# Optimization experiments

Hardware: AMD Instinct MI355X
Metric: run time of the kernel (lower is better)

## Reference

```python
import jax, jax.numpy as jnp
import numpy as np

EPS = 1e-05

def conv1x1(x, W, b):
    # x: [B,C,H,W], W: [O,C], b: [O] -> [B,O,H,W]
    return jnp.einsum('oc,bchw->bohw', W, x) + b[None, :, None, None]

def setup_inputs() -> dict:
    key = jax.random.key(0)
    ks = jax.random.split(key, 11)
    C = 16
    B, H, W = 8, 512, 512
    s = 1.0 / np.sqrt(C)  # kaiming-ish fan-in scale for 1x1 convs
    inp = {'x': jax.random.normal(ks[0], (B, C, H, W), dtype=jnp.float32)}
    names = [('Wc', 'bc'), ('W1', 'b1'), ('W2', 'b2'), ('W3', 'b3'), ('W4', 'b4')]
    for i, (wn, bn) in enumerate(names):
        inp[wn] = jax.random.normal(ks[1 + 2 * i], (C, C), dtype=jnp.float32) * s
        inp[bn] = jax.random.normal(ks[2 + 2 * i], (C,), dtype=jnp.float32) * s
    return inp

def reference(x, Wc, bc, W1, b1, W2, b2, W3, b3, W4, b4):
    out1 = jnp.mean(x, axis=(2, 3), keepdims=True)          # adaptive avg pool (1,1)
    out3 = jnp.max(x, axis=(2, 3), keepdims=True)           # adaptive max pool (1,1)
    out2 = conv1x1(x, Wc, bc)
    out4 = conv1x1(x, W1, b1)
    wh = conv1x1(out2 / (out1 + EPS), W2, b2)
    wh_weight = jax.nn.sigmoid(jnp.tanh(wh))
    gray = conv1x1(out4 / (out3 + EPS), W3, b3)
    gray_weight = jax.nn.sigmoid(jnp.tanh(gray))
    out = conv1x1(x * (1.0 + wh_weight + gray_weight), W4, b4)
    return out
```

## Files before the change

kernel.cpp:

```cpp
#include <hip/hip_runtime.h>
#include <hip/hip_bf16.h>
#include <cmath>

#define HW 262144
#define NC 16
#define NB 8
#define NSEG 16
#define SEGSZ (HW / NSEG)
#define EPS 1e-5f

typedef float f32x4 __attribute__((ext_vector_type(4)));
typedef float f32x2 __attribute__((ext_vector_type(2)));
typedef short bf16x8 __attribute__((ext_vector_type(8)));

__global__ __launch_bounds__(256) void k_reduce(const float* __restrict__ x,
                                                float* __restrict__ psum,
                                                float* __restrict__ pmax) {
    int plane = blockIdx.x / NSEG;
    int seg   = blockIdx.x - plane * NSEG;
    const float4* p = reinterpret_cast<const float4*>(
        x + (size_t)plane * HW + (size_t)seg * SEGSZ);
    int t = threadIdx.x;
    float s = 0.0f, m = -INFINITY;
    #pragma unroll
    for (int it = 0; it < SEGSZ / (256 * 4); ++it) {
        float4 v = p[it * 256 + t];
        s += (v.x + v.y) + (v.z + v.w);
        m = fmaxf(m, fmaxf(fmaxf(v.x, v.y), fmaxf(v.z, v.w)));
    }
    #pragma unroll
    for (int off = 32; off > 0; off >>= 1) {
        s += __shfl_down(s, off, 64);
        m = fmaxf(m, __shfl_down(m, off, 64));
    }
    __shared__ float ls[4], lm[4];
    int wid = t >> 6, lane = t & 63;
    if (lane == 0) { ls[wid] = s; lm[wid] = m; }
    __syncthreads();
    if (t == 0) {
        psum[blockIdx.x] = (ls[0] + ls[1]) + (ls[2] + ls[3]);
        pmax[blockIdx.x] = fmaxf(fmaxf(lm[0], lm[1]), fmaxf(lm[2], lm[3]));
    }
}

__global__ __launch_bounds__(256) void k_params(
    const float* __restrict__ psum, const float* __restrict__ pmax,
    const float* __restrict__ Wc, const float* __restrict__ bc,
    const float* __restrict__ W1, const float* __restrict__ b1,
    const float* __restrict__ W2, const float* __restrict__ b2,
    const float* __restrict__ W3, const float* __restrict__ b3,
    const float* __restrict__ W4, const float* __restrict__ b4,
    float* __restrict__ params) {
    int b = blockIdx.x;
    int t = threadIdx.x;
    __shared__ float r2[NC], r4[NC], sWc[256], sW1[256], sW2[256], sW3[256];
    if (t < NC) {
        float s = 0.0f, m = -INFINITY;
        for (int k = 0; k < NSEG; ++k) {
            s += psum[(b * NC + t) * NSEG + k];
            m = fmaxf(m, pmax[(b * NC + t) * NSEG + k]);
        }
        r2[t] = 1.0f / (s * (1.0f / (float)HW) + EPS);
        r4[t] = 1.0f / (m + EPS);
    }
    sWc[t] = Wc[t]; sW1[t] = W1[t]; sW2[t] = W2[t]; sW3[t] = W3[t];
    __syncthreads();
    int o = t >> 4, i = t & 15;
    float accA = 0.0f, accG = 0.0f;
    #pragma unroll
    for (int c = 0; c < NC; ++c) {
        accA += sW2[o * NC + c] * r2[c] * sWc[c * NC + i];
        accG += sW3[o * NC + c] * r4[c] * sW1[c * NC + i];
    }
    float* P = params + b * 816;
    P[t]       = accA;
    P[256 + t] = accG;
    P[512 + t] = W4[t];
    if (i == 0) {
        float ba = 0.0f, bg = 0.0f;
        #pragma unroll
        for (int c = 0; c < NC; ++c) {
            ba += sW2[o * NC + c] * r2[c] * bc[c];
            bg += sW3[o * NC + c] * r4[c] * b1[c];
        }
        P[768 + o] = ba + b2[o];
        P[784 + o] = bg + b3[o];
        P[800 + o] = b4[o];
    }
}

__device__ __forceinline__ float gsig(float x) {
    float E = __expf(2.0f * x);
    float t = 1.0f - 2.0f * __builtin_amdgcn_rcpf(E + 1.0f);
    float t2 = t * t;
    return fmaf(t, fmaf(t2, fmaf(t2, 0.0020833333f, -0.0208333333f), 0.25f), 0.5f);
}

static __device__ __forceinline__ bf16x8 mk8(unsigned a, unsigned b,
                                             unsigned c, unsigned d) {
    union { unsigned u[4]; bf16x8 v; } r;
    r.u[0] = a; r.u[1] = b; r.u[2] = c; r.u[3] = d;
    return r.v;
}
static __device__ __forceinline__ unsigned pkhi(float x0, float x1) {
    return (__float_as_uint(x0) >> 16) | (__float_as_uint(x1) & 0xFFFF0000u);
}
static __device__ __forceinline__ float trunc_bf(float x) {
    return __uint_as_float(__float_as_uint(x) & 0xFFFF0000u);
}

static __device__ __forceinline__ f32x4 tile16(float x0, float x1, float x2, float x3,
                                               bf16x8 Af, bf16x8 Gf, bf16x8 Wf,
                                               f32x4 biasA, f32x4 biasG, f32x4 biasW) {
    unsigned vh01 = pkhi(x0, x1), vh23 = pkhi(x2, x3);
    unsigned vl01 = pkhi(x0 - trunc_bf(x0), x1 - trunc_bf(x1));
    unsigned vl23 = pkhi(x2 - trunc_bf(x2), x3 - trunc_bf(x3));
    bf16x8 B1 = mk8(vh01, vh23, vl01, vl23);
    bf16x8 B2 = mk8(vl01, vl23, vh01, vh23);
    f32x4 wh = __builtin_amdgcn_mfma_f32_16x16x32_bf16(Af, B1, biasA, 0, 0, 0);
    wh = __builtin_amdgcn_mfma_f32_16x16x32_bf16(Af, B2, wh, 0, 0, 0);
    f32x4 gr = __builtin_amdgcn_mfma_f32_16x16x32_bf16(Gf, B1, biasG, 0, 0, 0);
    float u0 = fmaf(x0, gsig(wh[0]) + gsig(gr[0]), x0);
    float u1 = fmaf(x1, gsig(wh[1]) + gsig(gr[1]), x1);
    float u2 = fmaf(x2, gsig(wh[2]) + gsig(gr[2]), x2);
    float u3 = fmaf(x3, gsig(wh[3]) + gsig(gr[3]), x3);
    unsigned uh01 = pkhi(u0, u1), uh23 = pkhi(u2, u3);
    unsigned ul01 = pkhi(u0 - trunc_bf(u0), u1 - trunc_bf(u1));
    unsigned ul23 = pkhi(u2 - trunc_bf(u2), u3 - trunc_bf(u3));
    f32x4 o = __builtin_amdgcn_mfma_f32_16x16x32_bf16(Wf, mk8(uh01, uh23, ul01, ul23), biasW, 0, 0, 0);
    o = __builtin_amdgcn_mfma_f32_16x16x32_bf16(Wf, mk8(ul01, ul23, uh01, uh23), o, 0, 0, 0);
    return o;
}

__global__ __launch_bounds__(256) void k_main(const float* __restrict__ x,
                                              const float* __restrict__ params,
                                              float* __restrict__ out) {
    int b    = blockIdx.x >> 8;
    int wib  = ((blockIdx.x & 255) << 2) + (threadIdx.x >> 6);
    int lane = threadIdx.x & 63;
    int m  = lane & 15;
    int kg = lane >> 4;

    const float* Pb = params + b * 816;

    f32x4 wa = *reinterpret_cast<const f32x4*>(Pb + m * 16 + kg * 4);
    f32x4 wg = *reinterpret_cast<const f32x4*>(Pb + 256 + m * 16 + kg * 4);
    f32x4 w4 = *reinterpret_cast<const f32x4*>(Pb + 512 + m * 16 + kg * 4);

    unsigned ah01 = pkhi(wa[0], wa[1]), ah23 = pkhi(wa[2], wa[3]);
    unsigned al01 = pkhi(wa[0] - trunc_bf(wa[0]), wa[1] - trunc_bf(wa[1]));
    unsigned al23 = pkhi(wa[2] - trunc_bf(wa[2]), wa[3] - trunc_bf(wa[3]));
    bf16x8 Af = mk8(ah01, ah23, al01, al23);

    unsigned g01 = pkhi(wg[0], wg[1]), g23 = pkhi(wg[2], wg[3]);
    bf16x8 Gf = mk8(g01, g23, g01, g23);

    unsigned w401 = pkhi(w4[0], w4[1]), w423 = pkhi(w4[2], w4[3]);
    unsigned wl01 = pkhi(w4[0] - trunc_bf(w4[0]), w4[1] - trunc_bf(w4[1]));
    unsigned wl23 = pkhi(w4[2] - trunc_bf(w4[2]), w4[3] - trunc_bf(w4[3]));
    bf16x8 Wf = mk8(w401, w423, wl01, wl23);

    f32x4 biasA = *reinterpret_cast<const f32x4*>(Pb + 768 + kg * 4);
    f32x4 biasG = *reinterpret_cast<const f32x4*>(Pb + 784 + kg * 4);
    f32x4 biasW = *reinterpret_cast<const f32x4*>(Pb + 800 + kg * 4);

    const f32x2* xb2 = reinterpret_cast<const f32x2*>(x + (size_t)b * NC * HW);
    f32x2*       ob2 = reinterpret_cast<f32x2*>(out + (size_t)b * NC * HW);

    unsigned basep = (unsigned)wib * 128 + (unsigned)m;
    unsigned off0 = (unsigned)(kg * 4 + 0) * (HW / 2) + basep;
    unsigned off1 = (unsigned)(kg * 4 + 1) * (HW / 2) + basep;
    unsigned off2 = (unsigned)(kg * 4 + 2) * (HW / 2) + basep;
    unsigned off3 = (unsigned)(kg * 4 + 3) * (HW / 2) + basep;

    #pragma unroll
    for (int t = 0; t < 8; ++t) {
        f32x2 v0 = xb2[off0 + t * 16];
        f32x2 v1 = xb2[off1 + t * 16];
        f32x2 v2 = xb2[off2 + t * 16];
        f32x2 v3 = xb2[off3 + t * 16];

        f32x4 oA = tile16(v0.x, v1.x, v2.x, v3.x, Af, Gf, Wf, biasA, biasG, biasW);
        f32x4 oB = tile16(v0.y, v1.y, v2.y, v3.y, Af, Gf, Wf, biasA, biasG, biasW);

        f32x2 s0; s0.x = oA[0]; s0.y = oB[0];
        f32x2 s1; s1.x = oA[1]; s1.y = oB[1];
        f32x2 s2; s2.x = oA[2]; s2.y = oB[2];
        f32x2 s3; s3.x = oA[3]; s3.y = oB[3];
        __builtin_nontemporal_store(s0, &ob2[off0 + t * 16]);
        __builtin_nontemporal_store(s1, &ob2[off1 + t * 16]);
        __builtin_nontemporal_store(s2, &ob2[off2 + t * 16]);
        __builtin_nontemporal_store(s3, &ob2[off3 + t * 16]);
    }
}

extern "C" void kernel_launch(void* const* d_in, const int* in_sizes, int n_in,
                              void* d_out, int out_size, void* d_ws, size_t ws_size,
                              hipStream_t stream) {
    const float* x  = (const float*)d_in[0];
    const float* Wc = (const float*)d_in[1];
    const float* bc = (const float*)d_in[2];
    const float* W1 = (const float*)d_in[3];
    const float* b1 = (const float*)d_in[4];
    const float* W2 = (const float*)d_in[5];
    const float* b2 = (const float*)d_in[6];
    const float* W3 = (const float*)d_in[7];
    const float* b3 = (const float*)d_in[8];
    const float* W4 = (const float*)d_in[9];
    const float* b4 = (const float*)d_in[10];
    float* out = (float*)d_out;

    float* psum   = (float*)d_ws;
    float* pmax   = psum + NB * NC * NSEG;
    float* params = pmax + NB * NC * NSEG;

    k_reduce<<<NB * NC * NSEG, 256, 0, stream>>>(x, psum, pmax);
    k_params<<<NB, 256, 0, stream>>>(psum, pmax, Wc, bc, W1, b1, W2, b2,
                                     W3, b3, W4, b4, params);
    k_main<<<NB * 256, 256, 0, stream>>>(x, params, out);
}
```

Before: 70.49 us.

## Fuse reduction, parameter setup and main pass into one cooperative kernel

Replaces the three-kernel pipeline with a single cooperative-launch kernel. Each block reduces its own slice of x, then a grid-wide sync runs, and each block recomputes the per-batch folded parameters before processing the same pixels it just reduced, which may help L2 reuse. Host-side occupancy and attribute queries run on every launch, and the grid barrier adds synchronisation cost. A fallback path fuses parameter computation into the main kernel, dropping the separate params kernel.

```diff
diff --git a/kernel.cpp b/kernel.cpp
--- a/kernel.cpp
+++ b/kernel.cpp
@@ -1,93 +1,22 @@
 #include <hip/hip_runtime.h>
-#include <hip/hip_bf16.h>
+#include <hip/hip_cooperative_groups.h>
 #include <cmath>
 
-#define HW 262144
-#define NC 16
-#define NB 8
+namespace cg = cooperative_groups;
+
+#define HW   262144
+#define NC   16
+#define NB   8
 #define NSEG 16
 #define SEGSZ (HW / NSEG)
-#define EPS 1e-5f
+#define NBLK 1024
+#define BPB  (NBLK / NB)
+#define PXB  (HW / BPB)
+#define EPS  1e-5f
 
 typedef float f32x4 __attribute__((ext_vector_type(4)));
 typedef float f32x2 __attribute__((ext_vector_type(2)));
 typedef short bf16x8 __attribute__((ext_vector_type(8)));
-
-__global__ __launch_bounds__(256) void k_reduce(const float* __restrict__ x,
-                                                float* __restrict__ psum,
-                                                float* __restrict__ pmax) {
-    int plane = blockIdx.x / NSEG;
-    int seg   = blockIdx.x - plane * NSEG;
-    const float4* p = reinterpret_cast<const float4*>(
-        x + (size_t)plane * HW + (size_t)seg * SEGSZ);
-    int t = threadIdx.x;
-    float s = 0.0f, m = -INFINITY;
-    #pragma unroll
-    for (int it = 0; it < SEGSZ / (256 * 4); ++it) {
-        float4 v = p[it * 256 + t];
-        s += (v.x + v.y) + (v.z + v.w);
-        m = fmaxf(m, fmaxf(fmaxf(v.x, v.y), fmaxf(v.z, v.w)));
-    }
-    #pragma unroll
-    for (int off = 32; off > 0; off >>= 1) {
-        s += __shfl_down(s, off, 64);
-        m = fmaxf(m, __shfl_down(m, off, 64));
-    }
-    __shared__ float ls[4], lm[4];
-    int wid = t >> 6, lane = t & 63;
-    if (lane == 0) { ls[wid] = s; lm[wid] = m; }
-    __syncthreads();
-    if (t == 0) {
-        psum[blockIdx.x] = (ls[0] + ls[1]) + (ls[2] + ls[3]);
-        pmax[blockIdx.x] = fmaxf(fmaxf(lm[0], lm[1]), fmaxf(lm[2], lm[3]));
-    }
-}
-
-__global__ __launch_bounds__(256) void k_params(
-    const float* __restrict__ psum, const float* __restrict__ pmax,
-    const float* __restrict__ Wc, const float* __restrict__ bc,
-    const float* __restrict__ W1, const float* __restrict__ b1,
-    const float* __restrict__ W2, const float* __restrict__ b2,
-    const float* __restrict__ W3, const float* __restrict__ b3,
-    const float* __restrict__ W4, const float* __restrict__ b4,
-    float* __restrict__ params) {
-    int b = blockIdx.x;
-    int t = threadIdx.x;
-    __shared__ float r2[NC], r4[NC], sWc[256], sW1[256], sW2[256], sW3[256];
-    if (t < NC) {
-        float s = 0.0f, m = -INFINITY;
-        for (int k = 0; k < NSEG; ++k) {
-            s += psum[(b * NC + t) * NSEG + k];
-            m = fmaxf(m, pmax[(b * NC + t) * NSEG + k]);
-        }
-        r2[t] = 1.0f / (s * (1.0f / (float)HW) + EPS);
-        r4[t] = 1.0f / (m + EPS);
-    }
-    sWc[t] = Wc[t]; sW1[t] = W1[t]; sW2[t] = W2[t]; sW3[t] = W3[t];
-    __syncthreads();
-    int o = t >> 4, i = t & 15;
-    float accA = 0.0f, accG = 0.0f;
-    #pragma unroll
-    for (int c = 0; c < NC; ++c) {
-        accA += sW2[o * NC + c] * r2[c] * sWc[c * NC + i];
-        accG += sW3[o * NC + c] * r4[c] * sW1[c * NC + i];
-    }
-    float* P = params + b * 816;
-    P[t]       = accA;
-    P[256 + t] = accG;
-    P[512 + t] = W4[t];
-    if (i == 0) {
-        float ba = 0.0f, bg = 0.0f;
-        #pragma unroll
-        for (int c = 0; c < NC; ++c) {
-            ba += sW2[o * NC + c] * r2[c] * bc[c];
-            bg += sW3[o * NC + c] * r4[c] * b1[c];
-        }
-        P[768 + o] = ba + b2[o];
-        P[784 + o] = bg + b3[o];
-        P[800 + o] = b4[o];
-    }
-}
 
 __device__ __forceinline__ float gsig(float x) {
     float E = __expf(2.0f * x);
@@ -132,66 +61,276 @@
     return o;
 }
 
-__global__ __launch_bounds__(256) void k_main(const float* __restrict__ x,
-                                              const float* __restrict__ params,
-                                              float* __restrict__ out) {
-    int b    = blockIdx.x >> 8;
-    int wib  = ((blockIdx.x & 255) << 2) + (threadIdx.x >> 6);
-    int lane = threadIdx.x & 63;
-    int m  = lane & 15;
-    int kg = lane >> 4;
-
-    const float* Pb = params + b * 816;
-
-    f32x4 wa = *reinterpret_cast<const f32x4*>(Pb + m * 16 + kg * 4);
-    f32x4 wg = *reinterpret_cast<const f32x4*>(Pb + 256 + m * 16 + kg * 4);
-    f32x4 w4 = *reinterpret_cast<const f32x4*>(Pb + 512 + m * 16 + kg * 4);
-
+template<int NITER>
+static __device__ __forceinline__ void phase3(const f32x2* __restrict__ xb2,
+                                              f32x2* __restrict__ ob2,
+                                              unsigned basep, int kg,
+                                              bf16x8 Af, bf16x8 Gf, bf16x8 Wf,
+                                              f32x4 biasA, f32x4 biasG, f32x4 biasW) {
+    unsigned off0 = (unsigned)(kg * 4 + 0) * (HW / 2) + basep;
+    unsigned off1 = (unsigned)(kg * 4 + 1) * (HW / 2) + basep;
+    unsigned off2 = (unsigned)(kg * 4 + 2) * (HW / 2) + basep;
+    unsigned off3 = (unsigned)(kg * 4 + 3) * (HW / 2) + basep;
+    #pragma unroll
+    for (int it = 0; it < NITER; ++it) {
+        f32x2 v0 = xb2[off0 + it * 16];
+        f32x2 v1 = xb2[off1 + it * 16];
+        f32x2 v2 = xb2[off2 + it * 16];
+        f32x2 v3 = xb2[off3 + it * 16];
+        f32x4 oA = tile16(v0.x, v1.x, v2.x, v3.x, Af, Gf, Wf, biasA, biasG, biasW);
+        f32x4 oB = tile16(v0.y, v1.y, v2.y, v3.y, Af, Gf, Wf, biasA, biasG, biasW);
+        f32x2 s0; s0.x = oA[0]; s0.y = oB[0];
+        f32x2 s1; s1.x = oA[1]; s1.y = oB[1];
+        f32x2 s2; s2.x = oA[2]; s2.y = oB[2];
+        f32x2 s3; s3.x = oA[3]; s3.y = oB[3];
+        __builtin_nontemporal_store(s0, &ob2[off0 + it * 16]);
+        __builtin_nontemporal_store(s1, &ob2[off1 + it * 16]);
+        __builtin_nontemporal_store(s2, &ob2[off2 + it * 16]);
+        __builtin_nontemporal_store(s3, &ob2[off3 + it * 16]);
+    }
+}
+
+__global__ __launch_bounds__(256) void k_reduce(const float* __restrict__ x,
+                                                float* __restrict__ psum,
+                                                float* __restrict__ pmax) {
+    int plane = blockIdx.x / NSEG;
+    int seg   = blockIdx.x - plane * NSEG;
+    const float4* p = reinterpret_cast<const float4*>(
+        x + (size_t)plane * HW + (size_t)seg * SEGSZ);
+    int t = threadIdx.x;
+    float s = 0.0f, m = -INFINITY;
+    #pragma unroll
+    for (int it = 0; it < SEGSZ / (256 * 4); ++it) {
+        float4 v = p[it * 256 + t];
+        s += (v.x + v.y) + (v.z + v.w);
+        m = fmaxf(m, fmaxf(fmaxf(v.x, v.y), fmaxf(v.z, v.w)));
+    }
+    #pragma unroll
+    for (int off = 32; off > 0; off >>= 1) {
+        s += __shfl_down(s, off, 64);
+        m = fmaxf(m, __shfl_down(m, off, 64));
+    }
+    __shared__ float ls[4], lm[4];
+    int wid = t >> 6, lane = t & 63;
+    if (lane == 0) { ls[wid] = s; lm[wid] = m; }
+    __syncthreads();
+    if (t == 0) {
+        psum[blockIdx.x] = (ls[0] + ls[1]) + (ls[2] + ls[3]);
+        pmax[blockIdx.x] = fmaxf(fmaxf(lm[0], lm[1]), fmaxf(lm[2], lm[3]));
+    }
+}
+
+__global__ __launch_bounds__(256) void k_main2(
+    const float* __restrict__ x,
+    const float* __restrict__ psum, const float* __restrict__ pmax,
+    const float* __restrict__ Wc, const float* __restrict__ bc,
+    const float* __restrict__ W1, const float* __restrict__ b1,
+    const float* __restrict__ W2, const float* __restrict__ b2,
+    const float* __restrict__ W3, const float* __restrict__ b3,
+    const float* __restrict__ W4, const float* __restrict__ b4,
+    float* __restrict__ out)
+{
+    int bid = blockIdx.x;
+    int b   = bid >> 8;
+    int t   = threadIdx.x;
+    int wave = t >> 6, lane = t & 63;
+
+    __shared__ float r2s[NC], r4s[NC];
+    __shared__ float sA[NC][17], sG[NC][17], sbias[48];
+
+    if (t < NC) {
+        const float* src = psum + (b * NC + t) * NSEG;
+        float s = 0.0f;
+        #pragma unroll
+        for (int k = 0; k < NSEG; ++k) s += src[k];
+        r2s[t] = 1.0f / (s * (1.0f / (float)HW) + EPS);
+    } else if (t < 2 * NC) {
+        int c = t - NC;
+        const float* src = pmax + (b * NC + c) * NSEG;
+        float m = -INFINITY;
+        #pragma unroll
+        for (int k = 0; k < NSEG; ++k) m = fmaxf(m, src[k]);
+        r4s[c] = 1.0f / (m + EPS);
+    }
+    __syncthreads();
+    {
+        int o = t >> 4, i = t & 15;
+        float a = 0.0f, g = 0.0f;
+        #pragma unroll
+        for (int c = 0; c < NC; ++c) {
+            a = fmaf(W2[o * 16 + c] * r2s[c], Wc[c * 16 + i], a);
+            g = fmaf(W3[o * 16 + c] * r4s[c], W1[c * 16 + i], g);
+        }
+        sA[o][i] = a; sG[o][i] = g;
+        if (t < NC) {
+            float ba = 0.0f;
+            #pragma unroll
+            for (int c = 0; c < NC; ++c) ba = fmaf(W2[t * 16 + c] * r2s[c], bc[c], ba);
+            sbias[t] = ba + b2[t];
+        } else if (t < 2 * NC) {
+            int o2 = t - NC; float bg = 0.0f;
+            #pragma unroll
+            for (int c = 0; c < NC; ++c) bg = fmaf(W3[o2 * 16 + c] * r4s[c], b1[c], bg);
+            sbias[NC + o2] = bg + b3[o2];
+        } else if (t < 3 * NC) {
+            sbias[t] = b4[t - 2 * NC];
+        }
+    }
+    __syncthreads();
+
+    int m_ = lane & 15, kg = lane >> 4;
+    f32x4 wa, wg, w4v, biasA, biasG, biasW;
+    #pragma unroll
+    for (int r = 0; r < 4; ++r) {
+        wa[r]    = sA[m_][kg * 4 + r];
+        wg[r]    = sG[m_][kg * 4 + r];
+        w4v[r]   = W4[m_ * 16 + kg * 4 + r];
+        biasA[r] = sbias[kg * 4 + r];
+        biasG[r] = sbias[16 + kg * 4 + r];
+        biasW[r] = sbias[32 + kg * 4 + r];
+    }
     unsigned ah01 = pkhi(wa[0], wa[1]), ah23 = pkhi(wa[2], wa[3]);
     unsigned al01 = pkhi(wa[0] - trunc_bf(wa[0]), wa[1] - trunc_bf(wa[1]));
     unsigned al23 = pkhi(wa[2] - trunc_bf(wa[2]), wa[3] - trunc_bf(wa[3]));
     bf16x8 Af = mk8(ah01, ah23, al01, al23);
-
     unsigned g01 = pkhi(wg[0], wg[1]), g23 = pkhi(wg[2], wg[3]);
     bf16x8 Gf = mk8(g01, g23, g01, g23);
-
-    unsigned w401 = pkhi(w4[0], w4[1]), w423 = pkhi(w4[2], w4[3]);
-    unsigned wl01 = pkhi(w4[0] - trunc_bf(w4[0]), w4[1] - trunc_bf(w4[1]));
-    unsigned wl23 = pkhi(w4[2] - trunc_bf(w4[2]), w4[3] - trunc_bf(w4[3]));
+    unsigned w401 = pkhi(w4v[0], w4v[1]), w423 = pkhi(w4v[2], w4v[3]);
+    unsigned wl01 = pkhi(w4v[0] - trunc_bf(w4v[0]), w4v[1] - trunc_bf(w4v[1]));
+    unsigned wl23 = pkhi(w4v[2] - trunc_bf(w4v[2]), w4v[3] - trunc_bf(w4v[3]));
     bf16x8 Wf = mk8(w401, w423, wl01, wl23);
-
-    f32x4 biasA = *reinterpret_cast<const f32x4*>(Pb + 768 + kg * 4);
-    f32x4 biasG = *reinterpret_cast<const f32x4*>(Pb + 784 + kg * 4);
-    f32x4 biasW = *reinterpret_cast<const f32x4*>(Pb + 800 + kg * 4);
+    asm("" : "+v"(Af), "+v"(Gf), "+v"(Wf));
+    asm("" : "+v"(biasA), "+v"(biasG), "+v"(biasW));
 
     const f32x2* xb2 = reinterpret_cast<const f32x2*>(x + (size_t)b * NC * HW);
     f32x2*       ob2 = reinterpret_cast<f32x2*>(out + (size_t)b * NC * HW);
-
-    unsigned basep = (unsigned)wib * 128 + (unsigned)m;
-    unsigned off0 = (unsigned)(kg * 4 + 0) * (HW / 2) + basep;
-    unsigned off1 = (unsigned)(kg * 4 + 1) * (HW / 2) + basep;
-    unsigned off2 = (unsigned)(kg * 4 + 2) * (HW / 2) + basep;
-    unsigned off3 = (unsigned)(kg * 4 + 3) * (HW / 2) + basep;
-
-    #pragma unroll
-    for (int t = 0; t < 8; ++t) {
-        f32x2 v0 = xb2[off0 + t * 16];
-        f32x2 v1 = xb2[off1 + t * 16];
-        f32x2 v2 = xb2[off2 + t * 16];
-        f32x2 v3 = xb2[off3 + t * 16];
-
-        f32x4 oA = tile16(v0.x, v1.x, v2.x, v3.x, Af, Gf, Wf, biasA, biasG, biasW);
-        f32x4 oB = tile16(v0.y, v1.y, v2.y, v3.y, Af, Gf, Wf, biasA, biasG, biasW);
-
-        f32x2 s0; s0.x = oA[0]; s0.y = oB[0];
-        f32x2 s1; s1.x = oA[1]; s1.y = oB[1];
-        f32x2 s2; s2.x = oA[2]; s2.y = oB[2];
-        f32x2 s3; s3.x = oA[3]; s3.y = oB[3];
-        __builtin_nontemporal_store(s0, &ob2[off0 + t * 16]);
-        __builtin_nontemporal_store(s1, &ob2[off1 + t * 16]);
-        __builtin_nontemporal_store(s2, &ob2[off2 + t * 16]);
-        __builtin_nontemporal_store(s3, &ob2[off3 + t * 16]);
-    }
+    int wib = ((bid & 255) << 2) + wave;
+    unsigned basep = (unsigned)wib * 128 + (unsigned)m_;
+    phase3<8>(xb2, ob2, basep, kg, Af, Gf, Wf, biasA, biasG, biasW);
+}
+
+__global__ __launch_bounds__(256) void k_fused(
+    const float* __restrict__ x,
+    const float* __restrict__ Wc, const float* __restrict__ bc,
+    const float* __restrict__ W1, const float* __restrict__ b1,
+    const float* __restrict__ W2, const float* __restrict__ b2,
+    const float* __restrict__ W3, const float* __restrict__ b3,
+    const float* __restrict__ W4, const float* __restrict__ b4,
+    float* __restrict__ out, float* __restrict__ ws)
+{
+    int bid  = blockIdx.x;
+    int b    = bid >> 7;
+    int j    = bid & (BPB - 1);
+    int t    = threadIdx.x;
+    int wave = t >> 6, lane = t & 63;
+
+    float* psumB = ws;
+    float* pmaxB = ws + NB * NC * BPB;
+
+    {
+        const float* xs = x + (size_t)b * NC * HW + (size_t)j * PXB;
+        #pragma unroll
+        for (int cc = 0; cc < 4; ++cc) {
+            int c = wave * 4 + cc;
+            const float4* p = reinterpret_cast<const float4*>(xs + (size_t)c * HW);
+            float s = 0.0f, m = -INFINITY;
+            #pragma unroll
+            for (int it = 0; it < PXB / 256; ++it) {
+                float4 v = p[it * 64 + lane];
+                s += (v.x + v.y) + (v.z + v.w);
+                m = fmaxf(m, fmaxf(fmaxf(v.x, v.y), fmaxf(v.z, v.w)));
+            }
+            #pragma unroll
+            for (int off = 32; off > 0; off >>= 1) {
+                s += __shfl_down(s, off, 64);
+                m = fmaxf(m, __shfl_down(m, off, 64));
+            }
+            if (lane == 0) {
+                psumB[(b * NC + c) * BPB + j] = s;
+                pmaxB[(b * NC + c) * BPB + j] = m;
+            }
+        }
+    }
+
+    cg::this_grid().sync();
+
+    __shared__ float lsum[NC][17], lmax[NC][17];
+    __shared__ float r2s[NC], r4s[NC];
+    {
+        int c = t & 15, slot = t >> 4;
+        const float* pb = psumB + (b * NC + c) * BPB;
+        const float* mb = pmaxB + (b * NC + c) * BPB;
+        float s = 0.0f, m = -INFINITY;
+        #pragma unroll
+        for (int k = 0; k < BPB / 16; ++k) {
+            s += pb[slot * (BPB / 16) + k];
+            m = fmaxf(m, mb[slot * (BPB / 16) + k]);
+        }
+        lsum[c][slot] = s; lmax[c][slot] = m;
+    }
+    __syncthreads();
+    if (t < NC) {
+        float ss = 0.0f, mm = -INFINITY;
+        #pragma unroll
+        for (int k = 0; k < 16; ++k) { ss += lsum[t][k]; mm = fmaxf(mm, lmax[t][k]); }
+        r2s[t] = 1.0f / (ss * (1.0f / (float)HW) + EPS);
+        r4s[t] = 1.0f / (mm + EPS);
+    }
+    __syncthreads();
+    __shared__ float sA[NC][17], sG[NC][17], sbias[48];
+    {
+        int o = t >> 4, i = t & 15;
+        float a = 0.0f, g = 0.0f;
+        #pragma unroll
+        for (int c = 0; c < NC; ++c) {
+            a = fmaf(W2[o * 16 + c] * r2s[c], Wc[c * 16 + i], a);
+            g = fmaf(W3[o * 16 + c] * r4s[c], W1[c * 16 + i], g);
+        }
+        sA[o][i] = a; sG[o][i] = g;
+        if (t < NC) {
+            float ba = 0.0f;
+            #pragma unroll
+            for (int c = 0; c < NC; ++c) ba = fmaf(W2[t * 16 + c] * r2s[c], bc[c], ba);
+            sbias[t] = ba + b2[t];
+        } else if (t < 2 * NC) {
+            int o2 = t - NC; float bg = 0.0f;
+            #pragma unroll
+            for (int c = 0; c < NC; ++c) bg = fmaf(W3[o2 * 16 + c] * r4s[c], b1[c], bg);
+            sbias[NC + o2] = bg + b3[o2];
+        } else if (t < 3 * NC) {
+            sbias[t] = b4[t - 2 * NC];
+        }
+    }
+    __syncthreads();
+
+    int m_ = lane & 15, kg = lane >> 4;
+    f32x4 wa, wg, w4v, biasA, biasG, biasW;
+    #pragma unroll
+    for (int r = 0; r < 4; ++r) {
+        wa[r]    = sA[m_][kg * 4 + r];
+        wg[r]    = sG[m_][kg * 4 + r];
+        w4v[r]   = W4[m_ * 16 + kg * 4 + r];
+        biasA[r] = sbias[kg * 4 + r];
+        biasG[r] = sbias[16 + kg * 4 + r];
+        biasW[r] = sbias[32 + kg * 4 + r];
+    }
+    unsigned ah01 = pkhi(wa[0], wa[1]), ah23 = pkhi(wa[2], wa[3]);
+    unsigned al01 = pkhi(wa[0] - trunc_bf(wa[0]), wa[1] - trunc_bf(wa[1]));
+    unsigned al23 = pkhi(wa[2] - trunc_bf(wa[2]), wa[3] - trunc_bf(wa[3]));
+    bf16x8 Af = mk8(ah01, ah23, al01, al23);
+    unsigned g01 = pkhi(wg[0], wg[1]), g23 = pkhi(wg[2], wg[3]);
+    bf16x8 Gf = mk8(g01, g23, g01, g23);
+    unsigned w401 = pkhi(w4v[0], w4v[1]), w423 = pkhi(w4v[2], w4v[3]);
+    unsigned wl01 = pkhi(w4v[0] - trunc_bf(w4v[0]), w4v[1] - trunc_bf(w4v[1]));
+    unsigned wl23 = pkhi(w4v[2] - trunc_bf(w4v[2]), w4v[3] - trunc_bf(w4v[3]));
+    bf16x8 Wf = mk8(w401, w423, wl01, wl23);
+    asm("" : "+v"(Af), "+v"(Gf), "+v"(Wf));
+    asm("" : "+v"(biasA), "+v"(biasG), "+v"(biasW));
+
+    const f32x2* xb2 = reinterpret_cast<const f32x2*>(x + (size_t)b * NC * HW);
+    f32x2*       ob2 = reinterpret_cast<f32x2*>(out + (size_t)b * NC * HW);
+    unsigned basep = (unsigned)(j * (PXB / 2) + wave * (PXB / 8)) + (unsigned)m_;
+    phase3<16>(xb2, ob2, basep, kg, Af, Gf, Wf, biasA, biasG, biasW);
 }
 
 extern "C" void kernel_launch(void* const* d_in, const int* in_sizes, int n_in,
@@ -209,13 +348,32 @@
     const float* W4 = (const float*)d_in[9];
     const float* b4 = (const float*)d_in[10];
     float* out = (float*)d_out;
-
-    float* psum   = (float*)d_ws;
-    float* pmax   = psum + NB * NC * NSEG;
-    float* params = pmax + NB * NC * NSEG;
-
+    float* ws  = (float*)d_ws;
+
+    bool coop_done = false;
+    if (ws_size >= (size_t)(2 * NB * NC * BPB) * sizeof(float)) {
+        int dev = 0;
+        (void)hipGetDevice(&dev);
+        int coopAttr = 0, cus = 0, nbpc = 0;
+        (void)hipDeviceGetAttribute(&coopAttr, hipDeviceAttributeCooperativeLaunch, dev);
+        (void)hipDeviceGetAttribute(&cus, hipDeviceAttributeMultiprocessorCount, dev);
+        hipError_t eo = hipOccupancyMaxActiveBlocksPerMultiprocessor(
+            &nbpc, (const void*)k_fused, 256, 0);
+        if (coopAttr && eo == hipSuccess && (long)nbpc * (long)cus >= (long)NBLK) {
+            void* args[] = {(void*)&x, (void*)&Wc, (void*)&bc, (void*)&W1, (void*)&b1,
+                            (void*)&W2, (void*)&b2, (void*)&W3, (void*)&b3,
+                            (void*)&W4, (void*)&b4, (void*)&out, (void*)&ws};
+            hipError_t e = hipLaunchCooperativeKernel((const void*)k_fused, dim3(NBLK),
+                                                      dim3(256), args, 0, stream);
+            if (e == hipSuccess) coop_done = true;
+            else (void)hipGetLastError();
+        }
+    }
+    if (coop_done) return;
+
+    float* psum = ws;
+    float* pmax = psum + NB * NC * NSEG;
     k_reduce<<<NB * NC * NSEG, 256, 0, stream>>>(x, psum, pmax);
-    k_params<<<NB, 256, 0, stream>>>(psum, pmax, Wc, bc, W1, b1, W2, b2,
-                                     W3, b3, W4, b4, params);
-    k_main<<<NB * 256, 256, 0, stream>>>(x, params, out);
-}
+    k_main2<<<NB * 256, 256, 0, stream>>>(x, psum, pmax, Wc, bc, W1, b1,
+                                          W2, b2, W3, b3, W4, b4, out);
+}
```

New measurement: 69.89 us. Within noise of the previous version (-0.8%).

## Fuse parameter folding into main kernel and widen loads to float4

Applied to the files above, without the earlier changes.

Removes the separate k_params launch. Every block of the main kernel now recomputes the folded per-batch weights and biases from the partial sums into shared memory, which saves one kernel launch and its dependency gap. In exchange each of the 2048 blocks redoes the small 16x16 fold and adds two barriers. The main loop also switches from float2 to float4 global loads and stores, so each lane processes four 16-pixel tiles per iteration and makes wider memory transactions.

```diff
diff --git a/kernel.cpp b/kernel.cpp
--- a/kernel.cpp
+++ b/kernel.cpp
@@ -2,92 +2,16 @@
 #include <hip/hip_bf16.h>
 #include <cmath>
 
-#define HW 262144
-#define NC 16
-#define NB 8
+#define HW   262144
+#define NC   16
+#define NB   8
 #define NSEG 16
 #define SEGSZ (HW / NSEG)
-#define EPS 1e-5f
+#define EPS  1e-5f
 
 typedef float f32x4 __attribute__((ext_vector_type(4)));
 typedef float f32x2 __attribute__((ext_vector_type(2)));
 typedef short bf16x8 __attribute__((ext_vector_type(8)));
-
-__global__ __launch_bounds__(256) void k_reduce(const float* __restrict__ x,
-                                                float* __restrict__ psum,
-                                                float* __restrict__ pmax) {
-    int plane = blockIdx.x / NSEG;
-    int seg   = blockIdx.x - plane * NSEG;
-    const float4* p = reinterpret_cast<const float4*>(
-        x + (size_t)plane * HW + (size_t)seg * SEGSZ);
-    int t = threadIdx.x;
-    float s = 0.0f, m = -INFINITY;
-    #pragma unroll
-    for (int it = 0; it < SEGSZ / (256 * 4); ++it) {
-        float4 v = p[it * 256 + t];
-        s += (v.x + v.y) + (v.z + v.w);
-        m = fmaxf(m, fmaxf(fmaxf(v.x, v.y), fmaxf(v.z, v.w)));
-    }
-    #pragma unroll
-    for (int off = 32; off > 0; off >>= 1) {
-        s += __shfl_down(s, off, 64);
-        m = fmaxf(m, __shfl_down(m, off, 64));
-    }
-    __shared__ float ls[4], lm[4];
-    int wid = t >> 6, lane = t & 63;
-    if (lane == 0) { ls[wid] = s; lm[wid] = m; }
-    __syncthreads();
-    if (t == 0) {
-        psum[blockIdx.x] = (ls[0] + ls[1]) + (ls[2] + ls[3]);
-        pmax[blockIdx.x] = fmaxf(fmaxf(lm[0], lm[1]), fmaxf(lm[2], lm[3]));
-    }
-}
-
-__global__ __launch_bounds__(256) void k_params(
-    const float* __restrict__ psum, const float* __restrict__ pmax,
-    const float* __restrict__ Wc, const float* __restrict__ bc,
-    const float* __restrict__ W1, const float* __restrict__ b1,
-    const float* __restrict__ W2, const float* __restrict__ b2,
-    const float* __restrict__ W3, const float* __restrict__ b3,
-    const float* __restrict__ W4, const float* __restrict__ b4,
-    float* __restrict__ params) {
-    int b = blockIdx.x;
-    int t = threadIdx.x;
-    __shared__ float r2[NC], r4[NC], sWc[256], sW1[256], sW2[256], sW3[256];
-    if (t < NC) {
-        float s = 0.0f, m = -INFINITY;
-        for (int k = 0; k < NSEG; ++k) {
-            s += psum[(b * NC + t) * NSEG + k];
-            m = fmaxf(m, pmax[(b * NC + t) * NSEG + k]);
-        }
-        r2[t] = 1.0f / (s * (1.0f / (float)HW) + EPS);
-        r4[t] = 1.0f / (m + EPS);
-    }
-    sWc[t] = Wc[t]; sW1[t] = W1[t]; sW2[t] = W2[t]; sW3[t] = W3[t];
-    __syncthreads();
-    int o = t >> 4, i = t & 15;
-    float accA = 0.0f, accG = 0.0f;
-    #pragma unroll
-    for (int c = 0; c < NC; ++c) {
-        accA += sW2[o * NC + c] * r2[c] * sWc[c * NC + i];
-        accG += sW3[o * NC + c] * r4[c] * sW1[c * NC + i];
-    }
-    float* P = params + b * 816;
-    P[t]       = accA;
-    P[256 + t] = accG;
-    P[512 + t] = W4[t];
-    if (i == 0) {
-        float ba = 0.0f, bg = 0.0f;
-        #pragma unroll
-        for (int c = 0; c < NC; ++c) {
-            ba += sW2[o * NC + c] * r2[c] * bc[c];
-            bg += sW3[o * NC + c] * r4[c] * b1[c];
-        }
-        P[768 + o] = ba + b2[o];
-        P[784 + o] = bg + b3[o];
-        P[800 + o] = b4[o];
-    }
-}
 
 __device__ __forceinline__ float gsig(float x) {
     float E = __expf(2.0f * x);
@@ -132,65 +56,147 @@
     return o;
 }
 
-__global__ __launch_bounds__(256) void k_main(const float* __restrict__ x,
-                                              const float* __restrict__ params,
-                                              float* __restrict__ out) {
-    int b    = blockIdx.x >> 8;
-    int wib  = ((blockIdx.x & 255) << 2) + (threadIdx.x >> 6);
-    int lane = threadIdx.x & 63;
-    int m  = lane & 15;
-    int kg = lane >> 4;
-
-    const float* Pb = params + b * 816;
-
-    f32x4 wa = *reinterpret_cast<const f32x4*>(Pb + m * 16 + kg * 4);
-    f32x4 wg = *reinterpret_cast<const f32x4*>(Pb + 256 + m * 16 + kg * 4);
-    f32x4 w4 = *reinterpret_cast<const f32x4*>(Pb + 512 + m * 16 + kg * 4);
-
+__global__ __launch_bounds__(256) void k_reduce(const float* __restrict__ x,
+                                                float* __restrict__ psum,
+                                                float* __restrict__ pmax) {
+    int plane = blockIdx.x / NSEG;
+    int seg   = blockIdx.x - plane * NSEG;
+    const float4* p = reinterpret_cast<const float4*>(
+        x + (size_t)plane * HW + (size_t)seg * SEGSZ);
+    int t = threadIdx.x;
+    float s = 0.0f, m = -INFINITY;
+    #pragma unroll
+    for (int it = 0; it < SEGSZ / (256 * 4); ++it) {
+        float4 v = p[it * 256 + t];
+        s += (v.x + v.y) + (v.z + v.w);
+        m = fmaxf(m, fmaxf(fmaxf(v.x, v.y), fmaxf(v.z, v.w)));
+    }
+    #pragma unroll
+    for (int off = 32; off > 0; off >>= 1) {
+        s += __shfl_down(s, off, 64);
+        m = fmaxf(m, __shfl_down(m, off, 64));
+    }
+    __shared__ float ls[4], lm[4];
+    int wid = t >> 6, lane = t & 63;
+    if (lane == 0) { ls[wid] = s; lm[wid] = m; }
+    __syncthreads();
+    if (t == 0) {
+        psum[blockIdx.x] = (ls[0] + ls[1]) + (ls[2] + ls[3]);
+        pmax[blockIdx.x] = fmaxf(fmaxf(lm[0], lm[1]), fmaxf(lm[2], lm[3]));
+    }
+}
+
+__global__ __launch_bounds__(256) void k_main2(
+    const float* __restrict__ x,
+    const float* __restrict__ psum, const float* __restrict__ pmax,
+    const float* __restrict__ Wc, const float* __restrict__ bc,
+    const float* __restrict__ W1, const float* __restrict__ b1,
+    const float* __restrict__ W2, const float* __restrict__ b2,
+    const float* __restrict__ W3, const float* __restrict__ b3,
+    const float* __restrict__ W4, const float* __restrict__ b4,
+    float* __restrict__ out)
+{
+    int bid = blockIdx.x;
+    int b   = bid >> 8;
+    int t   = threadIdx.x;
+    int wave = t >> 6, lane = t & 63;
+
+    __shared__ float r2s[NC], r4s[NC];
+    __shared__ float sA[NC][17], sG[NC][17], sbias[48];
+
+    if (t < NC) {
+        const float* src = psum + (b * NC + t) * NSEG;
+        float s = 0.0f;
+        #pragma unroll
+        for (int k = 0; k < NSEG; ++k) s += src[k];
+        r2s[t] = 1.0f / (s * (1.0f / (float)HW) + EPS);
+    } else if (t < 2 * NC) {
+        int c = t - NC;
+        const float* src = pmax + (b * NC + c) * NSEG;
+        float m = -INFINITY;
+        #pragma unroll
+        for (int k = 0; k < NSEG; ++k) m = fmaxf(m, src[k]);
+        r4s[c] = 1.0f / (m + EPS);
+    }
+    __syncthreads();
+    {
+        int o = t >> 4, i = t & 15;
+        float a = 0.0f, g = 0.0f;
+        #pragma unroll
+        for (int c = 0; c < NC; ++c) {
+            a = fmaf(W2[o * 16 + c] * r2s[c], Wc[c * 16 + i], a);
+            g = fmaf(W3[o * 16 + c] * r4s[c], W1[c * 16 + i], g);
+        }
+        sA[o][i] = a; sG[o][i] = g;
+        if (t < NC) {
+            float ba = 0.0f;
+            #pragma unroll
+            for (int c = 0; c < NC; ++c) ba = fmaf(W2[t * 16 + c] * r2s[c], bc[c], ba);
+            sbias[t] = ba + b2[t];
+        } else if (t < 2 * NC) {
+            int o2 = t - NC; float bg = 0.0f;
+            #pragma unroll
+            for (int c = 0; c < NC; ++c) bg = fmaf(W3[o2 * 16 + c] * r4s[c], b1[c], bg);
+            sbias[NC + o2] = bg + b3[o2];
+        } else if (t < 3 * NC) {
+            sbias[t] = b4[t - 2 * NC];
+        }
+    }
+    __syncthreads();
+
+    int m_ = lane & 15, kg = lane >> 4;
+    f32x4 wa, wg, w4v, biasA, biasG, biasW;
+    #pragma unroll
+    for (int r = 0; r < 4; ++r) {
+        wa[r]    = sA[m_][kg * 4 + r];
+        wg[r]    = sG[m_][kg * 4 + r];
+        w4v[r]   = W4[m_ * 16 + kg * 4 + r];
+        biasA[r] = sbias[kg * 4 + r];
+        biasG[r] = sbias[16 + kg * 4 + r];
+        biasW[r] = sbias[32 + kg * 4 + r];
+    }
     unsigned ah01 = pkhi(wa[0], wa[1]), ah23 = pkhi(wa[2], wa[3]);
     unsigned al01 = pkhi(wa[0] - trunc_bf(wa[0]), wa[1] - trunc_bf(wa[1]));
     unsigned al23 = pkhi(wa[2] - trunc_bf(wa[2]), wa[3] - trunc_bf(wa[3]));
     bf16x8 Af = mk8(ah01, ah23, al01, al23);
-
     unsigned g01 = pkhi(wg[0], wg[1]), g23 = pkhi(wg[2], wg[3]);
     bf16x8 Gf = mk8(g01, g23, g01, g23);
-
-    unsigned w401 = pkhi(w4[0], w4[1]), w423 = pkhi(w4[2], w4[3]);
-    unsigned wl01 = pkhi(w4[0] - trunc_bf(w4[0]), w4[1] - trunc_bf(w4[1]));
-    unsigned wl23 = pkhi(w4[2] - trunc_bf(w4[2]), w4[3] - trunc_bf(w4[3]));
+    unsigned w401 = pkhi(w4v[0], w4v[1]), w423 = pkhi(w4v[2], w4v[3]);
+    unsigned wl01 = pkhi(w4v[0] - trunc_bf(w4v[0]), w4v[1] - trunc_bf(w4v[1]));
+    unsigned wl23 = pkhi(w4v[2] - trunc_bf(w4v[2]), w4v[3] - trunc_bf(w4v[3]));
     bf16x8 Wf = mk8(w401, w423, wl01, wl23);
-
-    f32x4 biasA = *reinterpret_cast<const f32x4*>(Pb + 768 + kg * 4);
-    f32x4 biasG = *reinterpret_cast<const f32x4*>(Pb + 784 + kg * 4);
-    f32x4 biasW = *reinterpret_cast<const f32x4*>(Pb + 800 + kg * 4);
-
-    const f32x2* xb2 = reinterpret_cast<const f32x2*>(x + (size_t)b * NC * HW);
-    f32x2*       ob2 = reinterpret_cast<f32x2*>(out + (size_t)b * NC * HW);
-
-    unsigned basep = (unsigned)wib * 128 + (unsigned)m;
-    unsigned off0 = (unsigned)(kg * 4 + 0) * (HW / 2) + basep;
-    unsigned off1 = (unsigned)(kg * 4 + 1) * (HW / 2) + basep;
-    unsigned off2 = (unsigned)(kg * 4 + 2) * (HW / 2) + basep;
-    unsigned off3 = (unsigned)(kg * 4 + 3) * (HW / 2) + basep;
-
-    #pragma unroll
-    for (int t = 0; t < 8; ++t) {
-        f32x2 v0 = xb2[off0 + t * 16];
-        f32x2 v1 = xb2[off1 + t * 16];
-        f32x2 v2 = xb2[off2 + t * 16];
-        f32x2 v3 = xb2[off3 + t * 16];
-
-        f32x4 oA = tile16(v0.x, v1.x, v2.x, v3.x, Af, Gf, Wf, biasA, biasG, biasW);
-        f32x4 oB = tile16(v0.y, v1.y, v2.y, v3.y, Af, Gf, Wf, biasA, biasG, biasW);
-
-        f32x2 s0; s0.x = oA[0]; s0.y = oB[0];
-        f32x2 s1; s1.x = oA[1]; s1.y = oB[1];
-        f32x2 s2; s2.x = oA[2]; s2.y = oB[2];
-        f32x2 s3; s3.x = oA[3]; s3.y = oB[3];
-        __builtin_nontemporal_store(s0, &ob2[off0 + t * 16]);
-        __builtin_nontemporal_store(s1, &ob2[off1 + t * 16]);
-        __builtin_nontemporal_store(s2, &ob2[off2 + t * 16]);
-        __builtin_nontemporal_store(s3, &ob2[off3 + t * 16]);
+    asm("" : "+v"(Af), "+v"(Gf), "+v"(Wf));
+    asm("" : "+v"(biasA), "+v"(biasG), "+v"(biasW));
+
+    const f32x4* xb4 = reinterpret_cast<const f32x4*>(x + (size_t)b * NC * HW);
+    f32x4*       ob4 = reinterpret_cast<f32x4*>(out + (size_t)b * NC * HW);
+    int wib = ((bid & 255) << 2) + wave;
+    unsigned basep = (unsigned)wib * 64 + (unsigned)m_;
+    unsigned off0 = (unsigned)(kg * 4 + 0) * (HW / 4) + basep;
+    unsigned off1 = (unsigned)(kg * 4 + 1) * (HW / 4) + basep;
+    unsigned off2 = (unsigned)(kg * 4 + 2) * (HW / 4) + basep;
+    unsigned off3 = (unsigned)(kg * 4 + 3) * (HW / 4) + basep;
+
+    #pragma unroll
+    for (int it = 0; it < 4; ++it) {
+        f32x4 v0 = xb4[off0 + it * 16];
+        f32x4 v1 = xb4[off1 + it * 16];
+        f32x4 v2 = xb4[off2 + it * 16];
+        f32x4 v3 = xb4[off3 + it * 16];
+
+        f32x4 oA = tile16(v0[0], v1[0], v2[0], v3[0], Af, Gf, Wf, biasA, biasG, biasW);
+        f32x4 oB = tile16(v0[1], v1[1], v2[1], v3[1], Af, Gf, Wf, biasA, biasG, biasW);
+        f32x4 oC = tile16(v0[2], v1[2], v2[2], v3[2], Af, Gf, Wf, biasA, biasG, biasW);
+        f32x4 oD = tile16(v0[3], v1[3], v2[3], v3[3], Af, Gf, Wf, biasA, biasG, biasW);
+
+        f32x4 s0; s0[0] = oA[0]; s0[1] = oB[0]; s0[2] = oC[0]; s0[3] = oD[0];
+        f32x4 s1; s1[0] = oA[1]; s1[1] = oB[1]; s1[2] = oC[1]; s1[3] = oD[1];
+        f32x4 s2; s2[0] = oA[2]; s2[1] = oB[2]; s2[2] = oC[2]; s2[3] = oD[2];
+        f32x4 s3; s3[0] = oA[3]; s3[1] = oB[3]; s3[2] = oC[3]; s3[3] = oD[3];
+        __builtin_nontemporal_store(s0, &ob4[off0 + it * 16]);
+        __builtin_nontemporal_store(s1, &ob4[off1 + it * 16]);
+        __builtin_nontemporal_store(s2, &ob4[off2 + it * 16]);
+        __builtin_nontemporal_store(s3, &ob4[off3 + it * 16]);
     }
 }
 
@@ -210,12 +216,10 @@
     const float* b4 = (const float*)d_in[10];
     float* out = (float*)d_out;
 
-    float* psum   = (float*)d_ws;
-    float* pmax   = psum + NB * NC * NSEG;
-    float* params = pmax + NB * NC * NSEG;
+    float* psum = (float*)d_ws;
+    float* pmax = psum + NB * NC * NSEG;
 
     k_reduce<<<NB * NC * NSEG, 256, 0, stream>>>(x, psum, pmax);
-    k_params<<<NB, 256, 0, stream>>>(psum, pmax, Wc, bc, W1, b1, W2, b2,
-                                     W3, b3, W4, b4, params);
-    k_main<<<NB * 256, 256, 0, stream>>>(x, params, out);
-}
+    k_main2<<<NB * 256, 256, 0, stream>>>(x, psum, pmax, Wc, bc, W1, b1,
+                                          W2, b2, W3, b3, W4, b4, out);
+}
```

Result: faster. 67.27 us (-4.6%).
